# Kernel tuning notes

Measured on AMD Instinct MI355X. Metric: run time of the kernel, lower is better.

## Reference

```python
import jax, jax.numpy as jnp
import numpy as np

D = 1024

def setup_inputs() -> dict:
    key = jax.random.key(0)
    ks = jax.random.split(key, 7)
    s = 1.0 / np.sqrt(D)
    return {
        "x": jax.random.normal(ks[0], (8, 2048, D), dtype=jnp.float32),
        "Wq": jax.random.uniform(ks[1], (D, D), jnp.float32, -s, s),
        "bq": jax.random.uniform(ks[2], (D,), jnp.float32, -s, s),
        "Wk": jax.random.uniform(ks[3], (D, D), jnp.float32, -s, s),
        "bk": jax.random.uniform(ks[4], (D,), jnp.float32, -s, s),
        "Wv": jax.random.uniform(ks[5], (D, D), jnp.float32, -s, s),
        "bv": jax.random.uniform(ks[6], (D,), jnp.float32, -s, s),
    }

def reference(x, Wq, bq, Wk, bk, Wv, bv):
    # torch Linear: y = x @ W.T + b
    Q = jnp.einsum('bsd,ed->bse', x, Wq) + bq
    K = jnp.einsum('bsd,ed->bse', x, Wk) + bk
    V = jnp.einsum('bsd,ed->bse', x, Wv) + bv
    scores = jnp.einsum('bse,bte->bst', Q, K) / jnp.sqrt(jnp.float32(x.shape[-1]))
    weights = jax.nn.softmax(scores, axis=-1)
    out = jnp.einsum('bst,bte->bse', weights, V)
    return jnp.mean(out, axis=0)
```

## Files before the change

### kernel.cpp

```cpp
#include <hip/hip_runtime.h>

typedef unsigned short u16;
typedef __attribute__((ext_vector_type(8))) short s16x8;
typedef __attribute__((ext_vector_type(4))) short s16x4;
typedef __attribute__((ext_vector_type(4))) float f32x4;

typedef const __attribute__((address_space(1))) void gas_void;
typedef __attribute__((address_space(3))) void las_void;

__device__ inline u16 f2bf(float f){
  union { float f; unsigned u; } c; c.f = f;
  unsigned r = c.u + 0x7fffu + ((c.u >> 16) & 1u);
  return (u16)(r >> 16);
}
__device__ inline float bf2f(u16 b){
  union { unsigned u; float f; } c; c.u = ((unsigned)b) << 16;
  return c.f;
}

extern "C" __global__ __launch_bounds__(256) void cvt_f32_bf16(
    const float* __restrict__ src, u16* __restrict__ dst, int n4){
  int stride = gridDim.x * blockDim.x;
  for (int i = blockIdx.x * blockDim.x + threadIdx.x; i < n4; i += stride){
    float4 f = reinterpret_cast<const float4*>(src)[i];
    s16x4 o;
    o[0] = (short)f2bf(f.x); o[1] = (short)f2bf(f.y);
    o[2] = (short)f2bf(f.z); o[3] = (short)f2bf(f.w);
    reinterpret_cast<s16x4*>(dst)[i] = o;
  }
}

extern "C" __global__ __launch_bounds__(256) void reduce8(
    const float* __restrict__ p, float* __restrict__ out, int n4, long stride4){
  int gs = gridDim.x * blockDim.x;
  for (int i = blockIdx.x * blockDim.x + threadIdx.x; i < n4; i += gs){
    float4 a = reinterpret_cast<const float4*>(p)[i];
    #pragma unroll
    for (int z = 1; z < 8; ++z){
      float4 b = reinterpret_cast<const float4*>(p)[i + z * stride4];
      a.x += b.x; a.y += b.y; a.z += b.z; a.w += b.w;
    }
    reinterpret_cast<float4*>(out)[i] = a;
  }
}

#define BM 256
#define BN 256
#define BK 64

__device__ inline void stage256(const u16* __restrict__ g, int ld, int row0, int k0,
                                u16* lds, int tid){
  const int wave = tid >> 6;
  #pragma unroll
  for (int j = 0; j < 4; ++j){
    int c = j * 512 + tid;
    int row = c >> 3, sch = c & 7;
    int ch = sch ^ (row & 7);
    const u16* src = g + (long)(row0 + row) * ld + k0 + ch * 8;
    u16* dst = lds + (size_t)(j * 512 + wave * 64) * 8;
    __builtin_amdgcn_global_load_lds((gas_void*)src, (las_void*)dst, 16, 0, 0);
  }
}

template<int EPI>
__global__ __launch_bounds__(512, 2) void gemm256(
    const u16* __restrict__ A, const u16* __restrict__ B, void* __restrict__ C,
    const float* __restrict__ bias, float scale, int K,
    int lda, int ldb, int ldc, long sAz, long sBz, long sCz)
{
  __shared__ u16 As[2][BM * BK];
  __shared__ u16 Bs[2][BN * BK];
  const int tid = threadIdx.x;
  const int lane = tid & 63, wave = tid >> 6;
  const int wm = (wave >> 2) * 128, wn = (wave & 3) * 64;

  const int gx = gridDim.x;
  const int nwg = gx * gridDim.y;
  const int hw = blockIdx.y * gx + blockIdx.x;
  const int lg = (hw & 7) * (nwg >> 3) + (hw >> 3);
  const int bm = (lg / gx) * BM, bn = (lg % gx) * BN;
  const int z = blockIdx.z;
  A += (long)z * sAz; B += (long)z * sBz;

  f32x4 acc[8][4];
  #pragma unroll
  for (int i = 0; i < 8; ++i)
    #pragma unroll
    for (int j = 0; j < 4; ++j) acc[i][j] = (f32x4){0.f, 0.f, 0.f, 0.f};

  const int lrow = lane & 15, lkg = lane >> 4;
  const int nt = K >> 6;

  auto compute = [&](const u16* as, const u16* bs){
    __builtin_amdgcn_s_setprio(1);
    #pragma unroll
    for (int kk = 0; kk < 2; ++kk){
      s16x8 bfr[4];
      #pragma unroll
      for (int j = 0; j < 4; ++j){
        int row = wn + j * 16 + lrow;
        int ch = (kk * 4 + lkg) ^ (row & 7);
        bfr[j] = *reinterpret_cast<const s16x8*>(
            reinterpret_cast<const char*>(bs) + row * 128 + ch * 16);
      }
      #pragma unroll
      for (int i = 0; i < 8; ++i){
        int row = wm + i * 16 + lrow;
        int ch = (kk * 4 + lkg) ^ (row & 7);
        s16x8 af = *reinterpret_cast<const s16x8*>(
            reinterpret_cast<const char*>(as) + row * 128 + ch * 16);
        #pragma unroll
        for (int j = 0; j < 4; ++j)
          acc[i][j] = __builtin_amdgcn_mfma_f32_16x16x32_bf16(af, bfr[j], acc[i][j], 0, 0, 0);
      }
    }
    __builtin_amdgcn_s_setprio(0);
  };

  stage256(A, lda, bm, 0, As[0], tid);
  stage256(B, ldb, bn, 0, Bs[0], tid);

  for (int t = 0; t < nt - 1; ++t){
    int nb = (t + 1) & 1;
    stage256(A, lda, bm, (t + 1) << 6, As[nb], tid);
    stage256(B, ldb, bn, (t + 1) << 6, Bs[nb], tid);
    asm volatile("s_waitcnt vmcnt(8)" ::: "memory");
    __builtin_amdgcn_s_barrier();
    asm volatile("" ::: "memory");
    compute(As[t & 1], Bs[t & 1]);
    asm volatile("" ::: "memory");
    __builtin_amdgcn_s_barrier();
    asm volatile("" ::: "memory");
  }
  asm volatile("s_waitcnt vmcnt(0)" ::: "memory");
  __builtin_amdgcn_s_barrier();
  asm volatile("" ::: "memory");
  compute(As[(nt - 1) & 1], Bs[(nt - 1) & 1]);

  #pragma unroll
  for (int i = 0; i < 8; ++i){
    #pragma unroll
    for (int j = 0; j < 4; ++j){
      #pragma unroll
      for (int r = 0; r < 4; ++r){
        int row = bm + wm + i * 16 + lkg * 4 + r;
        int col = bn + wn + j * 16 + lrow;
        float v = acc[i][j][r] * scale;
        if (EPI == 0){
          if (bias) v += bias[col];
          reinterpret_cast<u16*>(C)[(long)z * sCz + (long)row * ldc + col] = f2bf(v);
        } else if (EPI == 1){
          if (bias) v += bias[col];
          int b = row >> 11, t = row & 2047;
          reinterpret_cast<u16*>(C)[((long)b << 21) + ((long)col << 11) + t] = f2bf(v);
        } else {
          reinterpret_cast<float*>(C)[(long)z * sCz + (long)row * ldc + col] = v;
        }
      }
    }
  }
}

extern "C" __global__ __launch_bounds__(256) void softmax_rows(u16* __restrict__ S){
  long row = blockIdx.x;
  u16* p = S + row * 2048;
  int tid = threadIdx.x;
  s16x8 vv = reinterpret_cast<s16x8*>(p)[tid];
  float v[8];
  float m = -3.4e38f;
  #pragma unroll
  for (int j = 0; j < 8; ++j){ v[j] = bf2f((u16)vv[j]); m = fmaxf(m, v[j]); }
  #pragma unroll
  for (int o = 32; o; o >>= 1) m = fmaxf(m, __shfl_xor(m, o));
  __shared__ float sm[4], ss[4];
  int wave = tid >> 6, lane = tid & 63;
  if (lane == 0) sm[wave] = m;
  __syncthreads();
  m = fmaxf(fmaxf(sm[0], sm[1]), fmaxf(sm[2], sm[3]));
  float e[8], s = 0.f;
  #pragma unroll
  for (int j = 0; j < 8; ++j){ e[j] = __expf(v[j] - m); s += e[j]; }
  #pragma unroll
  for (int o = 32; o; o >>= 1) s += __shfl_xor(s, o);
  if (lane == 0) ss[wave] = s;
  __syncthreads();
  s = ss[0] + ss[1] + ss[2] + ss[3];
  float inv = 1.0f / s;
  s16x8 ov;
  #pragma unroll
  for (int j = 0; j < 8; ++j) ov[j] = (short)f2bf(e[j] * inv);
  reinterpret_cast<s16x8*>(p)[tid] = ov;
}

extern "C" void kernel_launch(void* const* d_in, const int* in_sizes, int n_in,
                              void* d_out, int out_size, void* d_ws, size_t ws_size,
                              hipStream_t stream){
  const float* x  = (const float*)d_in[0];
  const float* Wq = (const float*)d_in[1];
  const float* bq = (const float*)d_in[2];
  const float* Wk = (const float*)d_in[3];
  const float* bk = (const float*)d_in[4];
  const float* Wv = (const float*)d_in[5];
  const float* bv = (const float*)d_in[6];

  const long NX = 16384L * 1024;
  const long NW = 1024L * 1024;
  const long NS = 8L * 2048 * 2048;

  u16* xbf = (u16*)d_ws;
  u16* Wb  = xbf + NX;
  u16* Qb  = Wb + 3 * NW;
  u16* Kb  = Qb + NX;
  u16* Vtb = Kb + NX;
  u16* S   = Vtb + NX;

  float* partial = (float*)Qb;

  size_t need = (size_t)(NX + 3 * NW + 3 * NX + NS) * 2;
  if (ws_size < need) return;

  cvt_f32_bf16<<<2048, 256, 0, stream>>>(x, xbf, (int)(NX / 4));
  cvt_f32_bf16<<<512, 256, 0, stream>>>(Wq, Wb,           (int)(NW / 4));
  cvt_f32_bf16<<<512, 256, 0, stream>>>(Wk, Wb + NW,      (int)(NW / 4));
  cvt_f32_bf16<<<512, 256, 0, stream>>>(Wv, Wb + 2 * NW,  (int)(NW / 4));

  gemm256<0><<<dim3(4, 64, 1), 512, 0, stream>>>(
      xbf, Wb,          Qb,  bq, 1.f, 1024, 1024, 1024, 1024, 0, 0, 0);
  gemm256<0><<<dim3(4, 64, 1), 512, 0, stream>>>(
      xbf, Wb + NW,     Kb,  bk, 1.f, 1024, 1024, 1024, 1024, 0, 0, 0);
  gemm256<1><<<dim3(4, 64, 1), 512, 0, stream>>>(
      xbf, Wb + 2 * NW, Vtb, bv, 1.f, 1024, 1024, 1024, 0,    0, 0, 0);

  gemm256<0><<<dim3(8, 8, 8), 512, 0, stream>>>(
      Qb, Kb, S, nullptr, 0.03125f, 1024, 1024, 1024, 2048,
      2048L * 1024, 2048L * 1024, 2048L * 2048);

  softmax_rows<<<8 * 2048, 256, 0, stream>>>(S);

  gemm256<2><<<dim3(4, 8, 8), 512, 0, stream>>>(
      S, Vtb, partial, nullptr, 0.125f, 2048, 2048, 2048, 1024,
      2048L * 2048, 1024L * 2048, 2048L * 1024);

  reduce8<<<1024, 256, 0, stream>>>(
      partial, (float*)d_out, (int)(2048L * 1024 / 4), 2048L * 1024 / 4);
}
```

Measured before the change: 383.4 us.

## Split GEMM main loop into four phases interleaving LDS reads, staging and MFMA

Restructures the bf16 GEMM inner loop so each K tile is processed in four quarter-phases. A-fragment and B-fragment LDS reads for the next phase are issued between barriers, and the global-to-LDS prefetch of the next A and B tiles is split across phases. Each wave keeps only 4 A and 4 B fragments live, which cuts register pressure. The aim is to overlap LDS traffic and global loads with MFMA work in a ping-pong style schedule, at the cost of many more barriers per tile.

```diff
diff --git a/kernel.cpp b/kernel.cpp
--- a/kernel.cpp
+++ b/kernel.cpp
@@ -48,31 +48,20 @@
 #define BN 256
 #define BK 64
 
-__device__ inline void stage256(const u16* __restrict__ g, int ld, int row0, int k0,
-                                u16* lds, int tid){
-  const int wave = tid >> 6;
-  #pragma unroll
-  for (int j = 0; j < 4; ++j){
-    int c = j * 512 + tid;
-    int row = c >> 3, sch = c & 7;
-    int ch = sch ^ (row & 7);
-    const u16* src = g + (long)(row0 + row) * ld + k0 + ch * 8;
-    u16* dst = lds + (size_t)(j * 512 + wave * 64) * 8;
-    __builtin_amdgcn_global_load_lds((gas_void*)src, (las_void*)dst, 16, 0, 0);
-  }
-}
-
 template<int EPI>
 __global__ __launch_bounds__(512, 2) void gemm256(
     const u16* __restrict__ A, const u16* __restrict__ B, void* __restrict__ C,
     const float* __restrict__ bias, float scale, int K,
     int lda, int ldb, int ldc, long sAz, long sBz, long sCz)
 {
-  __shared__ u16 As[2][BM * BK];
-  __shared__ u16 Bs[2][BN * BK];
+  __shared__ u16 As[2][2][128 * 64];
+  __shared__ u16 Bs[2][2][128 * 64];
   const int tid = threadIdx.x;
   const int lane = tid & 63, wave = tid >> 6;
   const int wm = (wave >> 2) * 128, wn = (wave & 3) * 64;
+  const int ah = wm >> 7;
+  const int bh = wn >> 7;
+  const int wnh = wn & 127;
 
   const int gx = gridDim.x;
   const int nwg = gx * gridDim.y;
@@ -91,51 +80,122 @@
   const int lrow = lane & 15, lkg = lane >> 4;
   const int nt = K >> 6;
 
-  auto compute = [&](const u16* as, const u16* bs){
+  auto stage = [&](const u16* g, int ld, int row0, u16* base, int k0){
+    #pragma unroll
+    for (int l = 0; l < 2; ++l){
+      int c = l * 512 + tid;
+      int row = c >> 3, sch = c & 7;
+      int ch = sch ^ (row & 7);
+      const u16* src = g + (long)(row0 + row) * ld + k0 + ch * 8;
+      u16* dst = base + (size_t)(l * 512 + wave * 64) * 8;
+      __builtin_amdgcn_global_load_lds((gas_void*)src, (las_void*)dst, 16, 0, 0);
+    }
+  };
+  auto lda_f = [&](s16x8* d, const u16* base, int ih, int kk){
+    #pragma unroll
+    for (int i = 0; i < 4; ++i){
+      int rh = (ih * 4 + i) * 16 + lrow;
+      int ch = (kk * 4 + lkg) ^ (rh & 7);
+      d[i] = *reinterpret_cast<const s16x8*>(
+          reinterpret_cast<const char*>(base) + rh * 128 + ch * 16);
+    }
+  };
+  auto ldb_f = [&](s16x8* d, const u16* base, int kk){
+    #pragma unroll
+    for (int j = 0; j < 4; ++j){
+      int rh = wnh + j * 16 + lrow;
+      int ch = (kk * 4 + lkg) ^ (rh & 7);
+      d[j] = *reinterpret_cast<const s16x8*>(
+          reinterpret_cast<const char*>(base) + rh * 128 + ch * 16);
+    }
+  };
+
+  stage(A, lda, bm,       &As[0][0][0], 0);
+  stage(A, lda, bm + 128, &As[0][1][0], 0);
+  stage(B, ldb, bn,       &Bs[0][0][0], 0);
+  stage(B, ldb, bn + 128, &Bs[0][1][0], 0);
+
+  for (int t = 0; t < nt; ++t){
+    const int buf = t & 1, nbuf = buf ^ 1;
+    const u16* abase = &As[buf][ah][0];
+    const u16* bbase = &Bs[buf][bh][0];
+    const bool pf = (t + 1) < nt;
+    const int k1 = (t + 1) << 6;
+    s16x8 af[4], bfr[4];
+
+    if (pf){
+      stage(A, lda, bm,       &As[nbuf][0][0], k1);
+      stage(A, lda, bm + 128, &As[nbuf][1][0], k1);
+      asm volatile("s_waitcnt vmcnt(4)" ::: "memory");
+    } else {
+      asm volatile("s_waitcnt vmcnt(0)" ::: "memory");
+    }
+    __builtin_amdgcn_s_barrier();
+    asm volatile("" ::: "memory");
+    ldb_f(bfr, bbase, 0);
+    lda_f(af, abase, 0, 0);
+    asm volatile("s_waitcnt lgkmcnt(0)" ::: "memory");
+    __builtin_amdgcn_sched_barrier(0);
     __builtin_amdgcn_s_setprio(1);
     #pragma unroll
-    for (int kk = 0; kk < 2; ++kk){
-      s16x8 bfr[4];
-      #pragma unroll
-      for (int j = 0; j < 4; ++j){
-        int row = wn + j * 16 + lrow;
-        int ch = (kk * 4 + lkg) ^ (row & 7);
-        bfr[j] = *reinterpret_cast<const s16x8*>(
-            reinterpret_cast<const char*>(bs) + row * 128 + ch * 16);
-      }
-      #pragma unroll
-      for (int i = 0; i < 8; ++i){
-        int row = wm + i * 16 + lrow;
-        int ch = (kk * 4 + lkg) ^ (row & 7);
-        s16x8 af = *reinterpret_cast<const s16x8*>(
-            reinterpret_cast<const char*>(as) + row * 128 + ch * 16);
-        #pragma unroll
-        for (int j = 0; j < 4; ++j)
-          acc[i][j] = __builtin_amdgcn_mfma_f32_16x16x32_bf16(af, bfr[j], acc[i][j], 0, 0, 0);
-      }
-    }
+    for (int i = 0; i < 4; ++i)
+      #pragma unroll
+      for (int j = 0; j < 4; ++j)
+        acc[i][j] = __builtin_amdgcn_mfma_f32_16x16x32_bf16(af[i], bfr[j], acc[i][j], 0, 0, 0);
     __builtin_amdgcn_s_setprio(0);
-  };
-
-  stage256(A, lda, bm, 0, As[0], tid);
-  stage256(B, ldb, bn, 0, Bs[0], tid);
-
-  for (int t = 0; t < nt - 1; ++t){
-    int nb = (t + 1) & 1;
-    stage256(A, lda, bm, (t + 1) << 6, As[nb], tid);
-    stage256(B, ldb, bn, (t + 1) << 6, Bs[nb], tid);
-    asm volatile("s_waitcnt vmcnt(8)" ::: "memory");
-    __builtin_amdgcn_s_barrier();
-    asm volatile("" ::: "memory");
-    compute(As[t & 1], Bs[t & 1]);
-    asm volatile("" ::: "memory");
+    __builtin_amdgcn_s_barrier();
+    asm volatile("" ::: "memory");
+
+    lda_f(af, abase, 1, 0);
+    if (pf){
+      stage(B, ldb, bn,       &Bs[nbuf][0][0], k1);
+      stage(B, ldb, bn + 128, &Bs[nbuf][1][0], k1);
+    }
+    __builtin_amdgcn_s_barrier();
+    asm volatile("" ::: "memory");
+    asm volatile("s_waitcnt lgkmcnt(0)" ::: "memory");
+    __builtin_amdgcn_sched_barrier(0);
+    __builtin_amdgcn_s_setprio(1);
+    #pragma unroll
+    for (int i = 0; i < 4; ++i)
+      #pragma unroll
+      for (int j = 0; j < 4; ++j)
+        acc[4 + i][j] = __builtin_amdgcn_mfma_f32_16x16x32_bf16(af[i], bfr[j], acc[4 + i][j], 0, 0, 0);
+    __builtin_amdgcn_s_setprio(0);
+    __builtin_amdgcn_s_barrier();
+    asm volatile("" ::: "memory");
+
+    ldb_f(bfr, bbase, 1);
+    lda_f(af, abase, 0, 1);
+    __builtin_amdgcn_s_barrier();
+    asm volatile("" ::: "memory");
+    asm volatile("s_waitcnt lgkmcnt(0)" ::: "memory");
+    __builtin_amdgcn_sched_barrier(0);
+    __builtin_amdgcn_s_setprio(1);
+    #pragma unroll
+    for (int i = 0; i < 4; ++i)
+      #pragma unroll
+      for (int j = 0; j < 4; ++j)
+        acc[i][j] = __builtin_amdgcn_mfma_f32_16x16x32_bf16(af[i], bfr[j], acc[i][j], 0, 0, 0);
+    __builtin_amdgcn_s_setprio(0);
+    __builtin_amdgcn_s_barrier();
+    asm volatile("" ::: "memory");
+
+    lda_f(af, abase, 1, 1);
+    __builtin_amdgcn_s_barrier();
+    asm volatile("" ::: "memory");
+    asm volatile("s_waitcnt lgkmcnt(0)" ::: "memory");
+    __builtin_amdgcn_sched_barrier(0);
+    __builtin_amdgcn_s_setprio(1);
+    #pragma unroll
+    for (int i = 0; i < 4; ++i)
+      #pragma unroll
+      for (int j = 0; j < 4; ++j)
+        acc[4 + i][j] = __builtin_amdgcn_mfma_f32_16x16x32_bf16(af[i], bfr[j], acc[4 + i][j], 0, 0, 0);
+    __builtin_amdgcn_s_setprio(0);
     __builtin_amdgcn_s_barrier();
     asm volatile("" ::: "memory");
   }
-  asm volatile("s_waitcnt vmcnt(0)" ::: "memory");
-  __builtin_amdgcn_s_barrier();
-  asm volatile("" ::: "memory");
-  compute(As[(nt - 1) & 1], Bs[(nt - 1) & 1]);
 
   #pragma unroll
   for (int i = 0; i < 8; ++i){
@@ -151,8 +211,8 @@
           reinterpret_cast<u16*>(C)[(long)z * sCz + (long)row * ldc + col] = f2bf(v);
         } else if (EPI == 1){
           if (bias) v += bias[col];
-          int b = row >> 11, t = row & 2047;
-          reinterpret_cast<u16*>(C)[((long)b << 21) + ((long)col << 11) + t] = f2bf(v);
+          int b = row >> 11, tt = row & 2047;
+          reinterpret_cast<u16*>(C)[((long)b << 21) + ((long)col << 11) + tt] = f2bf(v);
         } else {
           reinterpret_cast<float*>(C)[(long)z * sCz + (long)row * ldc + col] = v;
         }
```

New measurement: 399.8 us. +4.3%, slower.

## Fuse Q/K/V projections into one GEMM and merge weight conversions

Applied to the files above, without the earlier changes.

The three weight conversions are merged into one kernel, and the three projection GEMMs become a single GEMM with N=3072 over concatenated weights. A new epilogue routes each column segment to Q, K or transposed V with its own bias. The tile-to-workgroup mapping is also changed to pair adjacent M tiles so neighbouring workgroups share B tiles. This is meant to remove launch overhead and tail effects from separate small GEMMs, and to improve cache reuse of x. The cost is a per-element branch in the epilogue and more complex index math.

```diff
diff --git a/kernel.cpp b/kernel.cpp
--- a/kernel.cpp
+++ b/kernel.cpp
@@ -30,6 +30,22 @@
   }
 }
 
+extern "C" __global__ __launch_bounds__(256) void cvt_w3(
+    const float* __restrict__ w0, const float* __restrict__ w1,
+    const float* __restrict__ w2, u16* __restrict__ dst, int n4each){
+  int stride = gridDim.x * blockDim.x;
+  int total = 3 * n4each;
+  for (int i = blockIdx.x * blockDim.x + threadIdx.x; i < total; i += stride){
+    int w = i / n4each, off = i - w * n4each;
+    const float* src = w == 0 ? w0 : w == 1 ? w1 : w2;
+    float4 f = reinterpret_cast<const float4*>(src)[off];
+    s16x4 o;
+    o[0] = (short)f2bf(f.x); o[1] = (short)f2bf(f.y);
+    o[2] = (short)f2bf(f.z); o[3] = (short)f2bf(f.w);
+    reinterpret_cast<s16x4*>(dst)[i] = o;
+  }
+}
+
 extern "C" __global__ __launch_bounds__(256) void reduce8(
     const float* __restrict__ p, float* __restrict__ out, int n4, long stride4){
   int gs = gridDim.x * blockDim.x;
@@ -65,7 +81,8 @@
 template<int EPI>
 __global__ __launch_bounds__(512, 2) void gemm256(
     const u16* __restrict__ A, const u16* __restrict__ B, void* __restrict__ C,
-    const float* __restrict__ bias, float scale, int K,
+    const float* __restrict__ bias, const float* __restrict__ bias2,
+    const float* __restrict__ bias3, float scale, int K,
     int lda, int ldb, int ldc, long sAz, long sBz, long sCz)
 {
   __shared__ u16 As[2][BM * BK];
@@ -78,7 +95,10 @@
   const int nwg = gx * gridDim.y;
   const int hw = blockIdx.y * gx + blockIdx.x;
   const int lg = (hw & 7) * (nwg >> 3) + (hw >> 3);
-  const int bm = (lg / gx) * BM, bn = (lg % gx) * BN;
+  const int pr  = lg / (2 * gx);
+  const int rem = lg - pr * 2 * gx;
+  const int bm = (pr * 2 + (rem & 1)) * BM;
+  const int bn = (rem >> 1) * BN;
   const int z = blockIdx.z;
   A += (long)z * sAz; B += (long)z * sBz;
 
@@ -151,10 +171,21 @@
           reinterpret_cast<u16*>(C)[(long)z * sCz + (long)row * ldc + col] = f2bf(v);
         } else if (EPI == 1){
           if (bias) v += bias[col];
-          int b = row >> 11, t = row & 2047;
-          reinterpret_cast<u16*>(C)[((long)b << 21) + ((long)col << 11) + t] = f2bf(v);
+          int b = row >> 11, tt = row & 2047;
+          reinterpret_cast<u16*>(C)[((long)b << 21) + ((long)col << 11) + tt] = f2bf(v);
+        } else if (EPI == 2){
+          reinterpret_cast<float*>(C)[(long)z * sCz + (long)row * ldc + col] = v;
         } else {
-          reinterpret_cast<float*>(C)[(long)z * sCz + (long)row * ldc + col] = v;
+          const long NXk = 16384L * 1024;
+          int seg = col >> 10, cb = col & 1023;
+          v += (seg == 0 ? bias : seg == 1 ? bias2 : bias3)[cb];
+          u16* Cb = reinterpret_cast<u16*>(C);
+          if (seg == 2){
+            int b = row >> 11, tt = row & 2047;
+            Cb[2 * NXk + ((long)b << 21) + ((long)cb << 11) + tt] = f2bf(v);
+          } else {
+            Cb[(long)seg * NXk + (long)row * 1024 + cb] = f2bf(v);
+          }
         }
       }
     }
@@ -220,25 +251,19 @@
   if (ws_size < need) return;
 
   cvt_f32_bf16<<<2048, 256, 0, stream>>>(x, xbf, (int)(NX / 4));
-  cvt_f32_bf16<<<512, 256, 0, stream>>>(Wq, Wb,           (int)(NW / 4));
-  cvt_f32_bf16<<<512, 256, 0, stream>>>(Wk, Wb + NW,      (int)(NW / 4));
-  cvt_f32_bf16<<<512, 256, 0, stream>>>(Wv, Wb + 2 * NW,  (int)(NW / 4));
-
-  gemm256<0><<<dim3(4, 64, 1), 512, 0, stream>>>(
-      xbf, Wb,          Qb,  bq, 1.f, 1024, 1024, 1024, 1024, 0, 0, 0);
-  gemm256<0><<<dim3(4, 64, 1), 512, 0, stream>>>(
-      xbf, Wb + NW,     Kb,  bk, 1.f, 1024, 1024, 1024, 1024, 0, 0, 0);
-  gemm256<1><<<dim3(4, 64, 1), 512, 0, stream>>>(
-      xbf, Wb + 2 * NW, Vtb, bv, 1.f, 1024, 1024, 1024, 0,    0, 0, 0);
+  cvt_w3<<<768, 256, 0, stream>>>(Wq, Wk, Wv, Wb, (int)(NW / 4));
+
+  gemm256<3><<<dim3(12, 64, 1), 512, 0, stream>>>(
+      xbf, Wb, Qb, bq, bk, bv, 1.f, 1024, 1024, 1024, 1024, 0, 0, 0);
 
   gemm256<0><<<dim3(8, 8, 8), 512, 0, stream>>>(
-      Qb, Kb, S, nullptr, 0.03125f, 1024, 1024, 1024, 2048,
+      Qb, Kb, S, nullptr, nullptr, nullptr, 0.03125f, 1024, 1024, 1024, 2048,
       2048L * 1024, 2048L * 1024, 2048L * 2048);
 
   softmax_rows<<<8 * 2048, 256, 0, stream>>>(S);
 
   gemm256<2><<<dim3(4, 8, 8), 512, 0, stream>>>(
-      S, Vtb, partial, nullptr, 0.125f, 2048, 2048, 2048, 1024,
+      S, Vtb, partial, nullptr, nullptr, nullptr, 0.125f, 2048, 2048, 2048, 1024,
       2048L * 2048, 1024L * 2048, 2048L * 1024);
 
   reduce8<<<1024, 256, 0, stream>>>(
```

Result: faster. 366.4 us (-4.4%).
